# Kernel tuning notes

Measured on AMD Instinct MI355X. Metric: run time of the kernel, lower is better.

## Reference

```python
import jax, jax.numpy as jnp
import numpy as np

NUM_HEADS = 16
BIG_NEG = -1e9  # additive mask value for padded keys (fp32)


def setup_inputs() -> dict:
    key = jax.random.key(0)
    ks = jax.random.split(key, 12)
    T, S, B, E = 2048, 2048, 2, 1024
    bound = np.sqrt(6.0 / (E + E))  # xavier_uniform for square E x E weights
    inp = {
        'query': jax.random.normal(ks[0], (T, B, E), jnp.float32),
        'key': jax.random.normal(ks[1], (S, B, E), jnp.float32),
        'value': jax.random.normal(ks[2], (S, B, E), jnp.float32),
        'attn_mask': jax.random.normal(ks[3], (T, S), jnp.float32) * 0.1,
        'key_padding_mask': jnp.zeros((B, S), dtype=bool),
        'Wq': jax.random.uniform(ks[4], (E, E), jnp.float32, -bound, bound),
        'bq': jnp.zeros((E,), jnp.float32),
        'Wk': jax.random.uniform(ks[5], (E, E), jnp.float32, -bound, bound),
        'bk': jnp.zeros((E,), jnp.float32),
        'Wv': jax.random.uniform(ks[6], (E, E), jnp.float32, -bound, bound),
        'bv': jnp.zeros((E,), jnp.float32),
        'Wo': jax.random.uniform(ks[7], (E, E), jnp.float32, -bound, bound),
        'bo': jnp.zeros((E,), jnp.float32),
    }
    return inp


def reference(query, key, value, attn_mask, key_padding_mask,
              Wq, bq, Wk, bk, Wv, bv, Wo, bo):
    T, B, E = query.shape
    S = key.shape[0]
    H = NUM_HEADS
    d = E // H
    scale = 1.0 / jnp.sqrt(jnp.asarray(d, query.dtype))

    # projections (nn.Linear: x @ W.T + b), then split heads
    q = (query @ Wq.T + bq).reshape(T, B, H, d) * scale  # [T,B,H,d]
    k = (key @ Wk.T + bk).reshape(S, B, H, d)            # [S,B,H,d]
    v = (value @ Wv.T + bv).reshape(S, B, H, d)          # [S,B,H,d]

    # QK^T scores: [B,H,T,S]
    scores = jnp.einsum('tbhd,sbhd->bhts', q, k)

    # merge masks: additive attn_mask + key_padding_mask (True -> -inf)
    merged = attn_mask[None, None, :, :] + jnp.where(
        key_padding_mask[:, None, None, :], BIG_NEG, 0.0).astype(scores.dtype)
    scores = scores + merged

    attn = jax.nn.softmax(scores, axis=-1)  # dropout p=0 -> identity

    out = jnp.einsum('bhts,sbhd->tbhd', attn, v).reshape(T, B, E)
    return out @ Wo.T + bo  # [T,B,E]
```

## Files before the change

kernel.cpp:

```cpp
#include <hip/hip_runtime.h>
#include <hip/hip_bf16.h>

typedef unsigned short u16;
typedef __attribute__((ext_vector_type(8))) short bf16x8;
typedef __attribute__((ext_vector_type(4))) float f32x4;

#define T_DIM 2048
#define S_DIM 2048
#define B_DIM 2
#define E_DIM 1024
#define H_DIM 16
#define D_HEAD 64
#define NTOK 4096

#if __has_builtin(__builtin_amdgcn_exp2f)
#define EXP2F(x) __builtin_amdgcn_exp2f(x)
#else
#define EXP2F(x) exp2f(x)
#endif

__device__ __forceinline__ float bf2f(u16 u) {
  union { unsigned int i; float f; } v; v.i = ((unsigned int)u) << 16; return v.f;
}
__device__ __forceinline__ u16 f2bf(float f) {
  union { float f; unsigned int i; } v; v.f = f;
  unsigned int r = v.i + 0x7fffu + ((v.i >> 16) & 1u);
  return (u16)(r >> 16);
}
__device__ __forceinline__ unsigned pk2(float a, float b) {
  return (unsigned)f2bf(a) | ((unsigned)f2bf(b) << 16);
}
__device__ __forceinline__ float bfu_lo(unsigned w) {
  union { unsigned int i; float f; } v; v.i = w << 16; return v.f;
}
__device__ __forceinline__ float bfu_hi(unsigned w) {
  union { unsigned int i; float f; } v; v.i = w & 0xffff0000u; return v.f;
}
__device__ __forceinline__ bf16x8 mk8(uint2 a, uint2 b) {
  union { uint4 u; bf16x8 v; } x;
  x.u = make_uint4(a.x, a.y, b.x, b.y);
  return x.v;
}
__device__ __forceinline__ uint4 loadA8(const void* A, size_t base, int bf) {
  if (bf) return *(const uint4*)&((const u16*)A)[base];
  const float* af = (const float*)A + base;
  uint4 r;
  r.x = pk2(af[0], af[1]); r.y = pk2(af[2], af[3]);
  r.z = pk2(af[4], af[5]); r.w = pk2(af[6], af[7]);
  return r;
}

__global__ void detect_dtype(const u16* q, int* flag) {
  int lane = threadIdx.x;
  float v = bf2f(q[2 * lane]);
  bool ok = (v < 16.f) && (v > -16.f);
  unsigned long long b = __ballot(ok);
  if (lane == 0) *flag = (b == ~0ull) ? 1 : 0;
}

__global__ void prep_params(const void* Wq, const void* Wk, const void* Wv, const void* Wo,
                            const void* bq, const void* bk, const void* bv, const void* bo,
                            u16* wqkv, u16* wo, float* b3, float* bof,
                            const int* flag) {
  const int bf = *flag;
  const int W = E_DIM * E_DIM;
  int idx = blockIdx.x * 256 + threadIdx.x;
  if (idx < 4 * W) {
    int which = idx / W, i = idx - which * W;
    const void* src = which == 0 ? Wq : which == 1 ? Wk : which == 2 ? Wv : Wo;
    float v = bf ? bf2f(((const u16*)src)[i]) : ((const float*)src)[i];
    if (which == 0) v *= 0.125f;
    if (which < 3) wqkv[idx] = f2bf(v);
    else           wo[i] = f2bf(v);
  } else {
    int j = idx - 4 * W;
    if (j < 4 * E_DIM) {
      int which = j / E_DIM, i = j - which * E_DIM;
      const void* src = which == 0 ? bq : which == 1 ? bk : which == 2 ? bv : bo;
      float v = bf ? bf2f(((const u16*)src)[i]) : ((const float*)src)[i];
      if (which == 0) v *= 0.125f;
      if (which < 3) b3[j] = v;
      else           bof[i] = v;
    }
  }
}

__global__ void prep_mask(const void* mask, const unsigned char* kpm,
                          u16* Mc, const int* flag) {
  const float L2E = 1.44269504f;
  const int bf = *flag;
  size_t e8 = ((size_t)blockIdx.x * 256 + threadIdx.x) * 8;
  int b = (int)(e8 / ((size_t)T_DIM * S_DIM));
  size_t rem = e8 - (size_t)b * T_DIM * S_DIM;
  int t = (int)(rem / S_DIM), s = (int)(rem - (size_t)t * S_DIM);
  const unsigned char* kb = &kpm[(size_t)b * S_DIM + s];
  uint4 o;
  if (bf) {
    const u16* m8 = &((const u16*)mask)[(size_t)t * S_DIM + s];
    o.x = pk2((bf2f(m8[0]) + (kb[0] ? -1e9f : 0.f)) * L2E,
              (bf2f(m8[1]) + (kb[1] ? -1e9f : 0.f)) * L2E);
    o.y = pk2((bf2f(m8[2]) + (kb[2] ? -1e9f : 0.f)) * L2E,
              (bf2f(m8[3]) + (kb[3] ? -1e9f : 0.f)) * L2E);
    o.z = pk2((bf2f(m8[4]) + (kb[4] ? -1e9f : 0.f)) * L2E,
              (bf2f(m8[5]) + (kb[5] ? -1e9f : 0.f)) * L2E);
    o.w = pk2((bf2f(m8[6]) + (kb[6] ? -1e9f : 0.f)) * L2E,
              (bf2f(m8[7]) + (kb[7] ? -1e9f : 0.f)) * L2E);
  } else {
    const float* mf = (const float*)mask + (size_t)t * S_DIM + s;
    o.x = pk2((mf[0] + (kb[0] ? -1e9f : 0.f)) * L2E,
              (mf[1] + (kb[1] ? -1e9f : 0.f)) * L2E);
    o.y = pk2((mf[2] + (kb[2] ? -1e9f : 0.f)) * L2E,
              (mf[3] + (kb[3] ? -1e9f : 0.f)) * L2E);
    o.z = pk2((mf[4] + (kb[4] ? -1e9f : 0.f)) * L2E,
              (mf[5] + (kb[5] ? -1e9f : 0.f)) * L2E);
    o.w = pk2((mf[6] + (kb[6] ? -1e9f : 0.f)) * L2E,
              (mf[7] + (kb[7] ? -1e9f : 0.f)) * L2E);
  }
  *(uint4*)&Mc[e8] = o;
}

__launch_bounds__(256)
__global__ void transpose_v(const u16* __restrict__ vp, u16* __restrict__ vt) {
  __shared__ unsigned int t[64 * 65];
  const int tid = threadIdx.x;
  const int s0 = blockIdx.x * 64;
  const int bh = blockIdx.y;
  const int b = bh / H_DIM, h = bh % H_DIM;
  {
    int sr = tid >> 2, cq = (tid & 3) * 16;
    const u16* src = &vp[((size_t)(s0 + sr) * B_DIM + b) * E_DIM + h * 64 + cq];
#pragma unroll
    for (int j = 0; j < 16; j++) t[(cq + j) * 65 + sr] = src[j];
  }
  __syncthreads();
  {
    int d = tid >> 2, sq = (tid & 3) * 16;
    u16* dst = &vt[((size_t)bh * 64 + d) * S_DIM + s0 + sq];
    uint4 o0, o1;
    o0.x = (t[d*65+sq+0] & 0xffffu) | (t[d*65+sq+1] << 16);
    o0.y = (t[d*65+sq+2] & 0xffffu) | (t[d*65+sq+3] << 16);
    o0.z = (t[d*65+sq+4] & 0xffffu) | (t[d*65+sq+5] << 16);
    o0.w = (t[d*65+sq+6] & 0xffffu) | (t[d*65+sq+7] << 16);
    o1.x = (t[d*65+sq+8] & 0xffffu) | (t[d*65+sq+9] << 16);
    o1.y = (t[d*65+sq+10] & 0xffffu) | (t[d*65+sq+11] << 16);
    o1.z = (t[d*65+sq+12] & 0xffffu) | (t[d*65+sq+13] << 16);
    o1.w = (t[d*65+sq+14] & 0xffffu) | (t[d*65+sq+15] << 16);
    *(uint4*)&dst[0] = o0;
    *(uint4*)&dst[8] = o1;
  }
}

__launch_bounds__(256, 2)
__global__ void gemm_qkv(const void* __restrict__ Qi, const void* __restrict__ Ki,
                         const void* __restrict__ Vi, const u16* __restrict__ W3,
                         const float* __restrict__ b3,
                         u16* __restrict__ qp, u16* __restrict__ kp, u16* __restrict__ vp,
                         const int* __restrict__ flag) {
  __shared__ alignas(16) u16 As[128 * 72];
  __shared__ alignas(16) u16 Bs[128 * 72];
  const int bf = *flag;
  const int tid = threadIdx.x;
  const int wave = tid >> 6, lane = tid & 63;
  const int g = lane >> 4, c = lane & 15;
  const int wy = wave >> 1, wx = wave & 1;
  const int which = blockIdx.x >> 3;
  const void* A = which == 0 ? Qi : which == 1 ? Ki : Vi;
  u16* dst = which == 0 ? qp : which == 1 ? kp : vp;
  const int m0 = blockIdx.y * 128, n0 = blockIdx.x * 128;
  const int K = E_DIM;
  const int rr = tid >> 3, oo = (tid & 7) * 8;

  uint4 pa0, pa1, pa2, pa3, pb0, pb1, pb2, pb3;
  pa0 = loadA8(A, (size_t)(m0 + rr)      * K + oo, bf);
  pa1 = loadA8(A, (size_t)(m0 + rr + 32) * K + oo, bf);
  pa2 = loadA8(A, (size_t)(m0 + rr + 64) * K + oo, bf);
  pa3 = loadA8(A, (size_t)(m0 + rr + 96) * K + oo, bf);
  pb0 = *(const uint4*)&W3[(size_t)(n0 + rr)      * K + oo];
  pb1 = *(const uint4*)&W3[(size_t)(n0 + rr + 32) * K + oo];
  pb2 = *(const uint4*)&W3[(size_t)(n0 + rr + 64) * K + oo];
  pb3 = *(const uint4*)&W3[(size_t)(n0 + rr + 96) * K + oo];

  f32x4 acc[4][4] = {};
  for (int kc = 0; kc < K; kc += 64) {
    *(uint4*)&As[(rr)      * 72 + oo] = pa0;
    *(uint4*)&As[(rr + 32) * 72 + oo] = pa1;
    *(uint4*)&As[(rr + 64) * 72 + oo] = pa2;
    *(uint4*)&As[(rr + 96) * 72 + oo] = pa3;
    *(uint4*)&Bs[(rr)      * 72 + oo] = pb0;
    *(uint4*)&Bs[(rr + 32) * 72 + oo] = pb1;
    *(uint4*)&Bs[(rr + 64) * 72 + oo] = pb2;
    *(uint4*)&Bs[(rr + 96) * 72 + oo] = pb3;
    __syncthreads();
    if (kc + 64 < K) {
      int k2 = kc + 64;
      pa0 = loadA8(A, (size_t)(m0 + rr)      * K + k2 + oo, bf);
      pa1 = loadA8(A, (size_t)(m0 + rr + 32) * K + k2 + oo, bf);
      pa2 = loadA8(A, (size_t)(m0 + rr + 64) * K + k2 + oo, bf);
      pa3 = loadA8(A, (size_t)(m0 + rr + 96) * K + k2 + oo, bf);
      pb0 = *(const uint4*)&W3[(size_t)(n0 + rr)      * K + k2 + oo];
      pb1 = *(const uint4*)&W3[(size_t)(n0 + rr + 32) * K + k2 + oo];
      pb2 = *(const uint4*)&W3[(size_t)(n0 + rr + 64) * K + k2 + oo];
      pb3 = *(const uint4*)&W3[(size_t)(n0 + rr + 96) * K + k2 + oo];
    }
#pragma unroll
    for (int ks = 0; ks < 2; ks++) {
      bf16x8 av0 = *(const bf16x8*)&As[(wy * 64 + 0 * 16 + c) * 72 + ks * 32 + g * 8];
      bf16x8 av1 = *(const bf16x8*)&As[(wy * 64 + 1 * 16 + c) * 72 + ks * 32 + g * 8];
      bf16x8 av2 = *(const bf16x8*)&As[(wy * 64 + 2 * 16 + c) * 72 + ks * 32 + g * 8];
      bf16x8 av3 = *(const bf16x8*)&As[(wy * 64 + 3 * 16 + c) * 72 + ks * 32 + g * 8];
      bf16x8 bv0 = *(const bf16x8*)&Bs[(wx * 64 + 0 * 16 + c) * 72 + ks * 32 + g * 8];
      bf16x8 bv1 = *(const bf16x8*)&Bs[(wx * 64 + 1 * 16 + c) * 72 + ks * 32 + g * 8];
      bf16x8 bv2 = *(const bf16x8*)&Bs[(wx * 64 + 2 * 16 + c) * 72 + ks * 32 + g * 8];
      bf16x8 bv3 = *(const bf16x8*)&Bs[(wx * 64 + 3 * 16 + c) * 72 + ks * 32 + g * 8];
      acc[0][0] = __builtin_amdgcn_mfma_f32_16x16x32_bf16(av0, bv0, acc[0][0], 0, 0, 0);
      acc[0][1] = __builtin_amdgcn_mfma_f32_16x16x32_bf16(av0, bv1, acc[0][1], 0, 0, 0);
      acc[0][2] = __builtin_amdgcn_mfma_f32_16x16x32_bf16(av0, bv2, acc[0][2], 0, 0, 0);
      acc[0][3] = __builtin_amdgcn_mfma_f32_16x16x32_bf16(av0, bv3, acc[0][3], 0, 0, 0);
      acc[1][0] = __builtin_amdgcn_mfma_f32_16x16x32_bf16(av1, bv0, acc[1][0], 0, 0, 0);
      acc[1][1] = __builtin_amdgcn_mfma_f32_16x16x32_bf16(av1, bv1, acc[1][1], 0, 0, 0);
      acc[1][2] = __builtin_amdgcn_mfma_f32_16x16x32_bf16(av1, bv2, acc[1][2], 0, 0, 0);
      acc[1][3] = __builtin_amdgcn_mfma_f32_16x16x32_bf16(av1, bv3, acc[1][3], 0, 0, 0);
      acc[2][0] = __builtin_amdgcn_mfma_f32_16x16x32_bf16(av2, bv0, acc[2][0], 0, 0, 0);
      acc[2][1] = __builtin_amdgcn_mfma_f32_16x16x32_bf16(av2, bv1, acc[2][1], 0, 0, 0);
      acc[2][2] = __builtin_amdgcn_mfma_f32_16x16x32_bf16(av2, bv2, acc[2][2], 0, 0, 0);
      acc[2][3] = __builtin_amdgcn_mfma_f32_16x16x32_bf16(av2, bv3, acc[2][3], 0, 0, 0);
      acc[3][0] = __builtin_amdgcn_mfma_f32_16x16x32_bf16(av3, bv0, acc[3][0], 0, 0, 0);
      acc[3][1] = __builtin_amdgcn_mfma_f32_16x16x32_bf16(av3, bv1, acc[3][1], 0, 0, 0);
      acc[3][2] = __builtin_amdgcn_mfma_f32_16x16x32_bf16(av3, bv2, acc[3][2], 0, 0, 0);
      acc[3][3] = __builtin_amdgcn_mfma_f32_16x16x32_bf16(av3, bv3, acc[3][3], 0, 0, 0);
    }
    __syncthreads();
  }
#pragma unroll
  for (int mi = 0; mi < 4; mi++)
#pragma unroll
    for (int ni = 0; ni < 4; ni++)
#pragma unroll
      for (int r = 0; r < 4; r++) {
        int row = m0 + wy * 64 + mi * 16 + g * 4 + r;
        int col = n0 + wx * 64 + ni * 16 + c;
        int inner = col & (E_DIM - 1);
        dst[(size_t)row * E_DIM + inner] = f2bf(acc[mi][ni][r] + b3[col]);
      }
}

__launch_bounds__(256, 2)
__global__ void gemm_o(const u16* __restrict__ A, const u16* __restrict__ Bw,
                       const float* __restrict__ bias, void* __restrict__ C,
                       int out_f32) {
  __shared__ alignas(16) u16 As[64 * 72];
  __shared__ alignas(16) u16 Bs[128 * 72];
  const int tid = threadIdx.x;
  const int wave = tid >> 6, lane = tid & 63;
  const int g = lane >> 4, c = lane & 15;
  const int wy = wave >> 1, wx = wave & 1;
  const int m0 = blockIdx.y * 64, n0 = blockIdx.x * 128;
  const int K = E_DIM, N = E_DIM;
  const int rr = tid >> 3, oo = (tid & 7) * 8;

  uint4 pa0, pa1, pb0, pb1, pb2, pb3;
  pa0 = *(const uint4*)&A[(size_t)(m0 + rr)      * K + oo];
  pa1 = *(const uint4*)&A[(size_t)(m0 + rr + 32) * K + oo];
  pb0 = *(const uint4*)&Bw[(size_t)(n0 + rr)      * K + oo];
  pb1 = *(const uint4*)&Bw[(size_t)(n0 + rr + 32) * K + oo];
  pb2 = *(const uint4*)&Bw[(size_t)(n0 + rr + 64) * K + oo];
  pb3 = *(const uint4*)&Bw[(size_t)(n0 + rr + 96) * K + oo];

  f32x4 acc[2][4] = {};
  for (int kc = 0; kc < K; kc += 64) {
    *(uint4*)&As[(rr)      * 72 + oo] = pa0;
    *(uint4*)&As[(rr + 32) * 72 + oo] = pa1;
    *(uint4*)&Bs[(rr)      * 72 + oo] = pb0;
    *(uint4*)&Bs[(rr + 32) * 72 + oo] = pb1;
    *(uint4*)&Bs[(rr + 64) * 72 + oo] = pb2;
    *(uint4*)&Bs[(rr + 96) * 72 + oo] = pb3;
    __syncthreads();
    if (kc + 64 < K) {
      int k2 = kc + 64;
      pa0 = *(const uint4*)&A[(size_t)(m0 + rr)      * K + k2 + oo];
      pa1 = *(const uint4*)&A[(size_t)(m0 + rr + 32) * K + k2 + oo];
      pb0 = *(const uint4*)&Bw[(size_t)(n0 + rr)      * K + k2 + oo];
      pb1 = *(const uint4*)&Bw[(size_t)(n0 + rr + 32) * K + k2 + oo];
      pb2 = *(const uint4*)&Bw[(size_t)(n0 + rr + 64) * K + k2 + oo];
      pb3 = *(const uint4*)&Bw[(size_t)(n0 + rr + 96) * K + k2 + oo];
    }
#pragma unroll
    for (int ks = 0; ks < 2; ks++) {
      bf16x8 av0 = *(const bf16x8*)&As[(wy * 32 + 0 * 16 + c) * 72 + ks * 32 + g * 8];
      bf16x8 av1 = *(const bf16x8*)&As[(wy * 32 + 1 * 16 + c) * 72 + ks * 32 + g * 8];
      bf16x8 bv0 = *(const bf16x8*)&Bs[(wx * 64 + 0 * 16 + c) * 72 + ks * 32 + g * 8];
      bf16x8 bv1 = *(const bf16x8*)&Bs[(wx * 64 + 1 * 16 + c) * 72 + ks * 32 + g * 8];
      bf16x8 bv2 = *(const bf16x8*)&Bs[(wx * 64 + 2 * 16 + c) * 72 + ks * 32 + g * 8];
      bf16x8 bv3 = *(const bf16x8*)&Bs[(wx * 64 + 3 * 16 + c) * 72 + ks * 32 + g * 8];
      acc[0][0] = __builtin_amdgcn_mfma_f32_16x16x32_bf16(av0, bv0, acc[0][0], 0, 0, 0);
      acc[0][1] = __builtin_amdgcn_mfma_f32_16x16x32_bf16(av0, bv1, acc[0][1], 0, 0, 0);
      acc[0][2] = __builtin_amdgcn_mfma_f32_16x16x32_bf16(av0, bv2, acc[0][2], 0, 0, 0);
      acc[0][3] = __builtin_amdgcn_mfma_f32_16x16x32_bf16(av0, bv3, acc[0][3], 0, 0, 0);
      acc[1][0] = __builtin_amdgcn_mfma_f32_16x16x32_bf16(av1, bv0, acc[1][0], 0, 0, 0);
      acc[1][1] = __builtin_amdgcn_mfma_f32_16x16x32_bf16(av1, bv1, acc[1][1], 0, 0, 0);
      acc[1][2] = __builtin_amdgcn_mfma_f32_16x16x32_bf16(av1, bv2, acc[1][2], 0, 0, 0);
      acc[1][3] = __builtin_amdgcn_mfma_f32_16x16x32_bf16(av1, bv3, acc[1][3], 0, 0, 0);
    }
    __syncthreads();
  }
#pragma unroll
  for (int mi = 0; mi < 2; mi++)
#pragma unroll
    for (int ni = 0; ni < 4; ni++)
#pragma unroll
      for (int r = 0; r < 4; r++) {
        int row = m0 + wy * 32 + mi * 16 + g * 4 + r;
        int col = n0 + wx * 64 + ni * 16 + c;
        float v = acc[mi][ni][r] + bias[col];
        size_t idx = (size_t)row * N + col;
        if (out_f32) ((float*)C)[idx] = v;
        else         ((u16*)C)[idx] = f2bf(v);
      }
}

#define STAGE(VSB) do {                                                        \
    *(uint4*)&Ks[(rr)      * 72 + oo] = pkA;                                   \
    *(uint4*)&Ks[(rr + 32) * 72 + oo] = pkB;                                   \
    *(uint4*)&(VSB)[(rr)      * 72 + oo] = pvA;                                \
    *(uint4*)&(VSB)[(rr + 32) * 72 + oo] = pvB;                                \
  } while (0)

#define PREFETCH(S2) do {                                                      \
    pkA = *(const uint4*)&Kb[((size_t)((S2) + rr)      * B_DIM + b) * E_DIM + hoff + oo]; \
    pkB = *(const uint4*)&Kb[((size_t)((S2) + rr + 32) * B_DIM + b) * E_DIM + hoff + oo]; \
    pvA = *(const uint4*)&Vtg[((size_t)bh * 64 + rr)      * S_DIM + (S2) + oo]; \
    pvB = *(const uint4*)&Vtg[((size_t)bh * 64 + rr + 32) * S_DIM + (S2) + oo]; \
  } while (0)

#define QKSOFT(PB, S0) do {                                                    \
    f32x4 sc[4] = {};                                                          \
    bf16x8 kf0 = *(const bf16x8*)&Ks[w16c * 72 + g * 8];                       \
    bf16x8 kf1 = *(const bf16x8*)&Ks[w16c * 72 + 32 + g * 8];                  \
    _Pragma("unroll")                                                          \
    for (int n = 0; n < 4; n++) {                                              \
      sc[n] = __builtin_amdgcn_mfma_f32_16x16x32_bf16(kf0, q[n][0], sc[n], 0, 0, 0); \
      sc[n] = __builtin_amdgcn_mfma_f32_16x16x32_bf16(kf1, q[n][1], sc[n], 0, 0, 0); \
    }                                                                          \
    _Pragma("unroll")                                                          \
    for (int n = 0; n < 4; n++) {                                              \
      uint2 mw = *(const uint2*)&mc[(size_t)(n * 16 + c) * S_DIM + (S0) + wS + g * 4]; \
      float p0 = EXP2F(fmaf(sc[n][0], L2E, bfu_lo(mw.x)));                     \
      float p1 = EXP2F(fmaf(sc[n][1], L2E, bfu_hi(mw.x)));                     \
      float p2 = EXP2F(fmaf(sc[n][2], L2E, bfu_lo(mw.y)));                     \
      float p3 = EXP2F(fmaf(sc[n][3], L2E, bfu_hi(mw.y)));                     \
      rs[n] += (p0 + p1) + (p2 + p3);                                          \
      PB[n] = make_uint2(pk2(p0, p1), pk2(p2, p3));                            \
    }                                                                          \
  } while (0)

__launch_bounds__(256, 2)
__global__ void flash_attn(const u16* __restrict__ Qb, const u16* __restrict__ Kb,
                           const u16* __restrict__ Vtg, const u16* __restrict__ Mc,
                           u16* __restrict__ ctx) {
  __shared__ alignas(16) u16 SH[3 * 64 * 72];
  u16* Ks  = SH;
  u16* Vs0 = SH + 4608;
  u16* Vs1 = SH + 2 * 4608;
  const int tid = threadIdx.x;
  const int wave = tid >> 6, lane = tid & 63;
  const int g = lane >> 4, c = lane & 15;
  const int bh = blockIdx.x;
  const int t0 = blockIdx.y * 64;
  const int b = bh / H_DIM, h = bh % H_DIM;
  const size_t hoff = (size_t)h * D_HEAD;
  const float L2E = 1.44269504f;
  const u16* mc = &Mc[((size_t)b * T_DIM + t0) * S_DIM];
  const int rr = tid >> 3, oo = (tid & 7) * 8;
  const int w16c = wave * 16 + c;
  const int wS   = wave * 16;

  *(uint4*)&Ks[(rr)      * 72 + oo] =
      *(const uint4*)&Qb[((size_t)(t0 + rr)      * B_DIM + b) * E_DIM + hoff + oo];
  *(uint4*)&Ks[(rr + 32) * 72 + oo] =
      *(const uint4*)&Qb[((size_t)(t0 + rr + 32) * B_DIM + b) * E_DIM + hoff + oo];
  __syncthreads();
  bf16x8 q[4][2];
#pragma unroll
  for (int n = 0; n < 4; n++) {
    q[n][0] = *(const bf16x8*)&Ks[(n * 16 + c) * 72 + g * 8];
    q[n][1] = *(const bf16x8*)&Ks[(n * 16 + c) * 72 + 32 + g * 8];
  }

  uint4 pkA, pkB, pvA, pvB;
  PREFETCH(0);
  __syncthreads();

  f32x4 o[4][4] = {};
  float rs[4] = {0.f, 0.f, 0.f, 0.f};
  uint2 pbA[4], pbB[4];

  for (int s0 = 0; s0 < S_DIM; s0 += 128) {
    STAGE(Vs0);
    __syncthreads();
    PREFETCH(s0 + 64);
    QKSOFT(pbA, s0);
    __syncthreads();
    STAGE(Vs1);
    __syncthreads();
    if (s0 + 128 < S_DIM) PREFETCH(s0 + 128);
    QKSOFT(pbB, s0 + 64);
#pragma unroll
    for (int m = 0; m < 4; m++) {
      uint2 va0 = *(const uint2*)&Vs0[(m * 16 + c) * 72 + wS + g * 4];
      uint2 vb0 = *(const uint2*)&Vs1[(m * 16 + c) * 72 + wS + g * 4];
      bf16x8 va = mk8(va0, vb0);
#pragma unroll
      for (int n = 0; n < 4; n++)
        o[m][n] = __builtin_amdgcn_mfma_f32_16x16x32_bf16(va, mk8(pbA[n], pbB[n]),
                                                          o[m][n], 0, 0, 0);
    }
    __syncthreads();
  }

  float l[4];
#pragma unroll
  for (int n = 0; n < 4; n++) {
    float x = rs[n];
    x += __shfl_xor(x, 16, 64);
    x += __shfl_xor(x, 32, 64);
    l[n] = x;
  }
  float* R  = (float*)SH;
  float* Rs = (float*)(SH + 2 * 4608);
  if (lane < 16) {
#pragma unroll
    for (int n = 0; n < 4; n++) Rs[wave * 64 + n * 16 + c] = l[n];
  }
  const int tt = tid >> 2, d4 = (tid & 3) * 4;
  u16* cp = &ctx[((size_t)(t0 + tt) * B_DIM + b) * E_DIM + hoff + d4];
  float rl = 0.f;
#pragma unroll
  for (int m = 0; m < 4; m++) {
#pragma unroll
    for (int n = 0; n < 4; n++)
      *(f32x4*)&R[wave * 1024 + (n * 16 + c) * 16 + g * 4] = o[m][n];
    __syncthreads();
    if (m == 0)
      rl = 1.f / (Rs[tt] + Rs[64 + tt] + Rs[128 + tt] + Rs[192 + tt]);
    f32x4 v0 = *(const f32x4*)&R[tt * 16 + d4];
    f32x4 v1 = *(const f32x4*)&R[1024 + tt * 16 + d4];
    f32x4 v2 = *(const f32x4*)&R[2048 + tt * 16 + d4];
    f32x4 v3 = *(const f32x4*)&R[3072 + tt * 16 + d4];
    f32x4 s = (v0 + v1) + (v2 + v3);
    *(uint2*)&cp[m * 16] = make_uint2(pk2(s[0] * rl, s[1] * rl),
                                      pk2(s[2] * rl, s[3] * rl));
    __syncthreads();
  }
}

extern "C" void kernel_launch(void* const* d_in, const int* in_sizes, int n_in,
                              void* d_out, int out_size, void* d_ws, size_t ws_size,
                              hipStream_t stream) {
  const void* query = d_in[0];
  const void* key   = d_in[1];
  const void* value = d_in[2];
  const void* amask = d_in[3];
  const unsigned char* kpm = (const unsigned char*)d_in[4];
  const void* Wq = d_in[5];  const void* bq = d_in[6];
  const void* Wk = d_in[7];  const void* bk = d_in[8];
  const void* Wv = d_in[9];  const void* bv = d_in[10];
  const void* Wo = d_in[11]; const void* bo = d_in[12];

  int out_f32 = 0;
  {
    hipDeviceptr_t base = nullptr; size_t sz = 0;
    if (hipMemGetAddressRange(&base, &sz, (hipDeviceptr_t)d_out) == hipSuccess && sz) {
      size_t avail = sz - (size_t)((char*)d_out - (char*)base);
      size_t need_f32 = (size_t)out_size * 4;
      if (avail >= need_f32 && avail <= need_f32 + need_f32 / 2) out_f32 = 1;
    }
  }

  char* ws = (char*)d_ws;
  size_t off = 0;
  auto alloc = [&](size_t bytes) {
    void* p = ws + off;
    off += (bytes + 255) & ~(size_t)255;
    return p;
  };
  int*   flag = (int*)  alloc(256);
  u16*   qp   = (u16*)  alloc((size_t)NTOK * E_DIM * 2);
  u16*   kp   = (u16*)  alloc((size_t)NTOK * E_DIM * 2);
  u16*   vp   = (u16*)  alloc((size_t)NTOK * E_DIM * 2);
  u16*   vt   = (u16*)  alloc((size_t)NTOK * E_DIM * 2);
  u16*   Mcb  = (u16*)  alloc((size_t)B_DIM * T_DIM * S_DIM * 2);
  u16*   wqkv = (u16*)  alloc((size_t)3 * E_DIM * E_DIM * 2);
  u16*   wo   = (u16*)  alloc((size_t)E_DIM * E_DIM * 2);
  float* b3   = (float*)alloc(3 * E_DIM * 4);
  float* bof  = (float*)alloc(E_DIM * 4);
  if (off > ws_size) return;

  detect_dtype<<<1, 64, 0, stream>>>((const u16*)query, flag);

  {
    int total = 4 * E_DIM * E_DIM + 4 * E_DIM;
    prep_params<<<(total + 255) / 256, 256, 0, stream>>>(
        Wq, Wk, Wv, Wo, bq, bk, bv, bo, wqkv, wo, b3, bof, flag);
  }
  {
    size_t total8 = (size_t)B_DIM * T_DIM * S_DIM / 8;
    prep_mask<<<(unsigned)(total8 / 256), 256, 0, stream>>>(amask, kpm, Mcb, flag);
  }

  gemm_qkv<<<dim3(3 * E_DIM / 128, NTOK / 128), 256, 0, stream>>>(
      query, key, value, wqkv, b3, qp, kp, vp, flag);

  transpose_v<<<dim3(S_DIM / 64, B_DIM * H_DIM), 256, 0, stream>>>(vp, vt);

  u16* ctx = vp;
  flash_attn<<<dim3(B_DIM * H_DIM, T_DIM / 64), 256, 0, stream>>>(qp, kp, vt, Mcb, ctx);

  gemm_o<<<dim3(E_DIM / 128, NTOK / 64), 256, 0, stream>>>(ctx, wo, bof, d_out, out_f32);
}
```

Baseline: 308.5 us.

## Halve flash-attention query tile to 32 rows and double-buffer K in LDS

Each flash-attention block now handles 32 query rows instead of 64. The grid doubles and the launch bound rises to 4 blocks per CU, which cuts per-thread accumulator and register use. K gets a second LDS buffer, so one barrier per 128-key iteration is removed. In exchange, every block re-reads the full K/V stream for half as many queries, doubling K/V global traffic, and the epilogue stores narrower output words.

```diff
diff --git a/kernel.cpp b/kernel.cpp
--- a/kernel.cpp
+++ b/kernel.cpp
@@ -318,9 +318,9 @@
       }
 }
 
-#define STAGE(VSB) do {                                                        \
-    *(uint4*)&Ks[(rr)      * 72 + oo] = pkA;                                   \
-    *(uint4*)&Ks[(rr + 32) * 72 + oo] = pkB;                                   \
+#define STAGE(KSB, VSB) do {                                                   \
+    *(uint4*)&(KSB)[(rr)      * 72 + oo] = pkA;                                \
+    *(uint4*)&(KSB)[(rr + 32) * 72 + oo] = pkB;                                \
     *(uint4*)&(VSB)[(rr)      * 72 + oo] = pvA;                                \
     *(uint4*)&(VSB)[(rr + 32) * 72 + oo] = pvB;                                \
   } while (0)
@@ -332,17 +332,17 @@
     pvB = *(const uint4*)&Vtg[((size_t)bh * 64 + rr + 32) * S_DIM + (S2) + oo]; \
   } while (0)
 
-#define QKSOFT(PB, S0) do {                                                    \
-    f32x4 sc[4] = {};                                                          \
-    bf16x8 kf0 = *(const bf16x8*)&Ks[w16c * 72 + g * 8];                       \
-    bf16x8 kf1 = *(const bf16x8*)&Ks[w16c * 72 + 32 + g * 8];                  \
+#define QKSOFT(PB, S0, KSB) do {                                               \
+    f32x4 sc[2] = {};                                                          \
+    bf16x8 kf0 = *(const bf16x8*)&(KSB)[w16c * 72 + g * 8];                    \
+    bf16x8 kf1 = *(const bf16x8*)&(KSB)[w16c * 72 + 32 + g * 8];               \
     _Pragma("unroll")                                                          \
-    for (int n = 0; n < 4; n++) {                                              \
+    for (int n = 0; n < 2; n++) {                                              \
       sc[n] = __builtin_amdgcn_mfma_f32_16x16x32_bf16(kf0, q[n][0], sc[n], 0, 0, 0); \
       sc[n] = __builtin_amdgcn_mfma_f32_16x16x32_bf16(kf1, q[n][1], sc[n], 0, 0, 0); \
     }                                                                          \
     _Pragma("unroll")                                                          \
-    for (int n = 0; n < 4; n++) {                                              \
+    for (int n = 0; n < 2; n++) {                                              \
       uint2 mw = *(const uint2*)&mc[(size_t)(n * 16 + c) * S_DIM + (S0) + wS + g * 4]; \
       float p0 = EXP2F(fmaf(sc[n][0], L2E, bfu_lo(mw.x)));                     \
       float p1 = EXP2F(fmaf(sc[n][1], L2E, bfu_hi(mw.x)));                     \
@@ -353,19 +353,20 @@
     }                                                                          \
   } while (0)
 
-__launch_bounds__(256, 2)
+__launch_bounds__(256, 4)
 __global__ void flash_attn(const u16* __restrict__ Qb, const u16* __restrict__ Kb,
                            const u16* __restrict__ Vtg, const u16* __restrict__ Mc,
                            u16* __restrict__ ctx) {
-  __shared__ alignas(16) u16 SH[3 * 64 * 72];
-  u16* Ks  = SH;
-  u16* Vs0 = SH + 4608;
-  u16* Vs1 = SH + 2 * 4608;
+  __shared__ alignas(16) u16 SH[4 * 64 * 72];
+  u16* Ks0 = SH;
+  u16* Ks1 = SH + 4608;
+  u16* Vs0 = SH + 2 * 4608;
+  u16* Vs1 = SH + 3 * 4608;
   const int tid = threadIdx.x;
   const int wave = tid >> 6, lane = tid & 63;
   const int g = lane >> 4, c = lane & 15;
   const int bh = blockIdx.x;
-  const int t0 = blockIdx.y * 64;
+  const int t0 = blockIdx.y * 32;
   const int b = bh / H_DIM, h = bh % H_DIM;
   const size_t hoff = (size_t)h * D_HEAD;
   const float L2E = 1.44269504f;
@@ -374,81 +375,78 @@
   const int w16c = wave * 16 + c;
   const int wS   = wave * 16;
 
-  *(uint4*)&Ks[(rr)      * 72 + oo] =
-      *(const uint4*)&Qb[((size_t)(t0 + rr)      * B_DIM + b) * E_DIM + hoff + oo];
-  *(uint4*)&Ks[(rr + 32) * 72 + oo] =
-      *(const uint4*)&Qb[((size_t)(t0 + rr + 32) * B_DIM + b) * E_DIM + hoff + oo];
+  *(uint4*)&Ks0[rr * 72 + oo] =
+      *(const uint4*)&Qb[((size_t)(t0 + rr) * B_DIM + b) * E_DIM + hoff + oo];
   __syncthreads();
-  bf16x8 q[4][2];
-#pragma unroll
-  for (int n = 0; n < 4; n++) {
-    q[n][0] = *(const bf16x8*)&Ks[(n * 16 + c) * 72 + g * 8];
-    q[n][1] = *(const bf16x8*)&Ks[(n * 16 + c) * 72 + 32 + g * 8];
+  bf16x8 q[2][2];
+#pragma unroll
+  for (int n = 0; n < 2; n++) {
+    q[n][0] = *(const bf16x8*)&Ks0[(n * 16 + c) * 72 + g * 8];
+    q[n][1] = *(const bf16x8*)&Ks0[(n * 16 + c) * 72 + 32 + g * 8];
   }
 
   uint4 pkA, pkB, pvA, pvB;
   PREFETCH(0);
   __syncthreads();
 
-  f32x4 o[4][4] = {};
-  float rs[4] = {0.f, 0.f, 0.f, 0.f};
-  uint2 pbA[4], pbB[4];
+  f32x4 o[4][2] = {};
+  float rs[2] = {0.f, 0.f};
+  uint2 pbA[2], pbB[2];
 
   for (int s0 = 0; s0 < S_DIM; s0 += 128) {
-    STAGE(Vs0);
+    STAGE(Ks0, Vs0);
     __syncthreads();
     PREFETCH(s0 + 64);
-    QKSOFT(pbA, s0);
-    __syncthreads();
-    STAGE(Vs1);
+    QKSOFT(pbA, s0, Ks0);
+    STAGE(Ks1, Vs1);
     __syncthreads();
     if (s0 + 128 < S_DIM) PREFETCH(s0 + 128);
-    QKSOFT(pbB, s0 + 64);
+    QKSOFT(pbB, s0 + 64, Ks1);
 #pragma unroll
     for (int m = 0; m < 4; m++) {
       uint2 va0 = *(const uint2*)&Vs0[(m * 16 + c) * 72 + wS + g * 4];
       uint2 vb0 = *(const uint2*)&Vs1[(m * 16 + c) * 72 + wS + g * 4];
       bf16x8 va = mk8(va0, vb0);
-#pragma unroll
-      for (int n = 0; n < 4; n++)
-        o[m][n] = __builtin_amdgcn_mfma_f32_16x16x32_bf16(va, mk8(pbA[n], pbB[n]),
-                                                          o[m][n], 0, 0, 0);
-    }
-    __syncthreads();
-  }
-
-  float l[4];
-#pragma unroll
-  for (int n = 0; n < 4; n++) {
+      o[m][0] = __builtin_amdgcn_mfma_f32_16x16x32_bf16(va, mk8(pbA[0], pbB[0]),
+                                                        o[m][0], 0, 0, 0);
+      o[m][1] = __builtin_amdgcn_mfma_f32_16x16x32_bf16(va, mk8(pbA[1], pbB[1]),
+                                                        o[m][1], 0, 0, 0);
+    }
+    __syncthreads();
+  }
+
+  float l[2];
+#pragma unroll
+  for (int n = 0; n < 2; n++) {
     float x = rs[n];
     x += __shfl_xor(x, 16, 64);
     x += __shfl_xor(x, 32, 64);
     l[n] = x;
   }
   float* R  = (float*)SH;
-  float* Rs = (float*)(SH + 2 * 4608);
+  float* Rs = (float*)(SH + 4096);
   if (lane < 16) {
-#pragma unroll
-    for (int n = 0; n < 4; n++) Rs[wave * 64 + n * 16 + c] = l[n];
-  }
-  const int tt = tid >> 2, d4 = (tid & 3) * 4;
-  u16* cp = &ctx[((size_t)(t0 + tt) * B_DIM + b) * E_DIM + hoff + d4];
+    Rs[wave * 32 + c]      = l[0];
+    Rs[wave * 32 + 16 + c] = l[1];
+  }
+  const int tt = tid >> 3, dq = (tid & 7) * 2;
+  u16* cp = &ctx[((size_t)(t0 + tt) * B_DIM + b) * E_DIM + hoff + dq];
   float rl = 0.f;
 #pragma unroll
   for (int m = 0; m < 4; m++) {
 #pragma unroll
-    for (int n = 0; n < 4; n++)
-      *(f32x4*)&R[wave * 1024 + (n * 16 + c) * 16 + g * 4] = o[m][n];
+    for (int n = 0; n < 2; n++)
+      *(f32x4*)&R[wave * 512 + (n * 16 + c) * 16 + g * 4] = o[m][n];
     __syncthreads();
     if (m == 0)
-      rl = 1.f / (Rs[tt] + Rs[64 + tt] + Rs[128 + tt] + Rs[192 + tt]);
-    f32x4 v0 = *(const f32x4*)&R[tt * 16 + d4];
-    f32x4 v1 = *(const f32x4*)&R[1024 + tt * 16 + d4];
-    f32x4 v2 = *(const f32x4*)&R[2048 + tt * 16 + d4];
-    f32x4 v3 = *(const f32x4*)&R[3072 + tt * 16 + d4];
-    f32x4 s = (v0 + v1) + (v2 + v3);
-    *(uint2*)&cp[m * 16] = make_uint2(pk2(s[0] * rl, s[1] * rl),
-                                      pk2(s[2] * rl, s[3] * rl));
+      rl = 1.f / (Rs[tt] + Rs[32 + tt] + Rs[64 + tt] + Rs[96 + tt]);
+    float2 v0 = *(const float2*)&R[tt * 16 + dq];
+    float2 v1 = *(const float2*)&R[512 + tt * 16 + dq];
+    float2 v2 = *(const float2*)&R[1024 + tt * 16 + dq];
+    float2 v3 = *(const float2*)&R[1536 + tt * 16 + dq];
+    float s0 = (v0.x + v1.x) + (v2.x + v3.x);
+    float s1 = (v0.y + v1.y) + (v2.y + v3.y);
+    *(unsigned*)&cp[m * 16] = pk2(s0 * rl, s1 * rl);
     __syncthreads();
   }
 }
@@ -513,7 +511,7 @@
   transpose_v<<<dim3(S_DIM / 64, B_DIM * H_DIM), 256, 0, stream>>>(vp, vt);
 
   u16* ctx = vp;
-  flash_attn<<<dim3(B_DIM * H_DIM, T_DIM / 64), 256, 0, stream>>>(qp, kp, vt, Mcb, ctx);
+  flash_attn<<<dim3(B_DIM * H_DIM, T_DIM / 32), 256, 0, stream>>>(qp, kp, vt, Mcb, ctx);
 
   gemm_o<<<dim3(E_DIM / 128, NTOK / 64), 256, 0, stream>>>(ctx, wo, bof, d_out, out_f32);
 }
```

Measured after the change: 331.9 us. 7.6% more time.
